# Performance work log

Hardware: AMD Instinct MI355X
Metric: run time of the kernel (lower is better)

Reference implementation:

```python
import jax, jax.numpy as jnp
import numpy as np

GATE_SLOPE = 10.0
ALPHA = 0.8
STRIDE = 1
PADDING = 1


def _unfold(x, kH, kW, stride, padding):
    # torch F.unfold equivalent, kept as (B, Cin, kH, kW, Hout, Wout)
    B, C, H, W = x.shape
    xp = jnp.pad(x, ((0, 0), (0, 0), (padding, padding), (padding, padding)))
    Hout = (H + 2 * padding - kH) // stride + 1
    Wout = (W + 2 * padding - kW) // stride + 1
    cols = []
    for i in range(kH):          # small fixed loop over kernel taps (9 iters)
        for j in range(kW):
            cols.append(xp[:, :, i:i + Hout * stride:stride, j:j + Wout * stride:stride])
    return jnp.stack(cols, axis=2).reshape(B, C, kH, kW, Hout, Wout)


def setup_inputs() -> dict:
    key = jax.random.key(0)
    ks = jax.random.split(key, 6)
    B, Cin, H, W = 4, 16, 32, 32
    Cout, K, kH, kW = 32, 3, 3, 3
    pshape = (Cout, Cin, K, kH, kW)
    x = jax.random.normal(ks[0], (B, Cin, H, W), jnp.float32)
    k = jax.random.uniform(ks[1], pshape, jnp.float32) * 2.0 + 0.5
    Ec = jax.random.uniform(ks[2], pshape, jnp.float32) * 2.0 + 0.5
    Ps = jax.random.uniform(ks[3], pshape, jnp.float32) * 1.5 + 0.5
    bias = jax.random.normal(ks[4], pshape, jnp.float32) * 0.1
    coef = jax.random.normal(ks[5], pshape, jnp.float32)
    out_bias = jnp.zeros((Cout,), jnp.float32)
    return {"x": x, "k": k, "Ec": Ec, "Ps": Ps, "bias": bias, "coef": coef, "out_bias": out_bias}


def reference(x, k, Ec, Ps, bias, coef, out_bias):
    kH, kW = k.shape[-2], k.shape[-1]
    patches = _unfold(x, kH, kW, STRIDE, PADDING)          # (B,Cin,kH,kW,Hout,Wout)
    # broadcast layout: (B, Cout, Cin, K, kH, kW, Hout, Wout)
    xe = patches[:, None, :, None]                          # (B,1,Cin,1,kH,kW,Ho,Wo)
    def bc(p):
        return p[None, :, :, :, :, :, None, None]
    k_, Ec_, Ps_, b_, c_ = bc(k), bc(Ec), bc(Ps), bc(bias), bc(coef)
    # stateless mode: prev_x = detach(x_exp) -> dx == 0 in value, grad flows via xe
    prev_x = jax.lax.stop_gradient(xe)
    is_moving_up = jax.nn.sigmoid(GATE_SLOPE * (xe - prev_x))
    crossed_pos = jax.nn.sigmoid(GATE_SLOPE * (xe - Ec_))
    crossed_neg = jax.nn.sigmoid(GATE_SLOPE * (-xe - Ec_))
    su = is_moving_up * crossed_pos
    sl = (1.0 - is_moving_up) * crossed_neg
    # branch_prev = +1 (stateless)
    target_sign = su - sl + (1.0 - su - sl)
    branch_mom = ALPHA + (1.0 - ALPHA) * target_sign
    shifted_x = xe + Ec_ * branch_mom
    basis = Ps_ * jnp.tanh(k_ * shifted_x) + b_
    out = jnp.sum(basis * c_, axis=(2, 3, 4, 5))            # (B,Cout,Hout,Wout)
    return out + out_bias[None, :, None, None]
```

## Files before the change

kernel.cpp:

```cpp
#include <hip/hip_runtime.h>


#define LOG2E 1.4426950408889634f

__global__ __launch_bounds__(256, 4) void ferro_kernel(
    const float* __restrict__ x, const float* __restrict__ k,
    const float* __restrict__ Ec, const float* __restrict__ Ps,
    const float* __restrict__ bias, const float* __restrict__ coef,
    const float* __restrict__ out_bias, float* __restrict__ out)
{
    const int bid = blockIdx.x;
    const int rb  = bid & 3;
    const int co  = (bid >> 2) & 31;
    const int b   = bid >> 7;
    const int tid = threadIdx.x;

    __shared__ float4 p4[432];
    __shared__ float  pA[432];
    __shared__ float  xs[16 * 10 * 34];
    __shared__ float  red[4];
    __shared__ float  constco_sh;

    const int pbase = co * 432;
    float cpart = 0.f;
    for (int s = tid; s < 432; s += 256) {
        float kv = k[pbase + s];
        float ev = Ec[pbase + s];
        float pv = Ps[pbase + s];
        float bv = bias[pbase + s];
        float cv = coef[pbase + s];
        float G  = 2.f * LOG2E * kv;
        float4 v;
        v.x = -10.f * LOG2E * ev;
        v.y = G;
        v.z = 0.8f * G * ev;
        v.w = 0.2f * G * ev;
        int cin = s / 27;
        int r   = s - cin * 27;
        int kk  = r / 9;
        int ij  = r - kk * 9;
        int dst = cin * 27 + ij * 3 + kk;
        p4[dst] = v;
        pA[dst] = -2.f * pv * cv;
        cpart += (pv + bv) * cv;
    }

    const int r0 = rb * 8;
    const float* xb = x + b * (16 * 32 * 32);
    for (int idx = tid; idx < 16 * 10 * 34; idx += 256) {
        int cin  = idx / 340;
        int rem  = idx - cin * 340;
        int row  = rem / 34;
        int colp = rem - row * 34;
        int gr = r0 + row - 1;
        int gc = colp - 1;
        float v = 0.f;
        if ((unsigned)gr < 32u && (unsigned)gc < 32u)
            v = xb[(cin * 32 + gr) * 32 + gc];
        xs[idx] = v;
    }

    #pragma unroll
    for (int off = 32; off > 0; off >>= 1)
        cpart += __shfl_down(cpart, off, 64);
    if ((tid & 63) == 0) red[tid >> 6] = cpart;
    __syncthreads();
    if (tid == 0) constco_sh = red[0] + red[1] + red[2] + red[3];
    __syncthreads();

    const int lr  = tid >> 5;
    const int col = tid & 31;
    const float Cx = -10.f * LOG2E;
    float acc = 0.f;

    #pragma unroll 2
    for (int cin = 0; cin < 16; ++cin) {
        const float*  xr = &xs[cin * 340 + lr * 34 + col];
        const float4* pp = &p4[cin * 27];
        const float*  aa = &pA[cin * 27];
        #pragma unroll
        for (int i = 0; i < 3; ++i) {
            #pragma unroll
            for (int j = 0; j < 3; ++j) {
                float xv = xr[i * 34 + j];
                float xC = Cx * xv;
                #pragma unroll
                for (int kk = 0; kk < 3; ++kk) {
                    int t = (i * 3 + j) * 3 + kk;
                    float4 v  = pp[t];
                    float  a2 = aa[t];
                    float e1 = __builtin_amdgcn_exp2f(xC + v.x);
                    float s  = __builtin_amdgcn_rcpf(e1 + 1.f);
                    float arg2 = fmaf(v.w, s, fmaf(v.y, xv, v.z));
                    float e2 = __builtin_amdgcn_exp2f(arg2);
                    float u  = __builtin_amdgcn_rcpf(e2 + 1.f);
                    acc = fmaf(a2, u, acc);
                }
            }
        }
    }

    float ob = out_bias[co];
    out[((b * 32 + co) * 32 + (r0 + lr)) * 32 + col] = constco_sh + acc + ob;
}

extern "C" void kernel_launch(void* const* d_in, const int* in_sizes, int n_in,
                              void* d_out, int out_size, void* d_ws, size_t ws_size,
                              hipStream_t stream) {
    const float* x        = (const float*)d_in[0];
    const float* k        = (const float*)d_in[1];
    const float* Ec       = (const float*)d_in[2];
    const float* Ps       = (const float*)d_in[3];
    const float* bias     = (const float*)d_in[4];
    const float* coef     = (const float*)d_in[5];
    const float* out_bias = (const float*)d_in[6];
    float* out = (float*)d_out;

    ferro_kernel<<<dim3(512), dim3(256), 0, stream>>>(
        x, k, Ec, Ps, bias, coef, out_bias, out);
}
```

Before: 97.04 us.

## Split parameter prep into separate kernel and split Cin across blocks with atomics

Moves per-output-channel parameter preprocessing and the constant term into a prep kernel that writes transformed parameters to workspace and initializes the output with the constant plus bias. The main kernel now splits the input channels in half across blocks, doubling the grid to 1024 blocks, and accumulates partial sums with atomicAdd. It also uses two accumulators to shorten the FMA dependency chain. This aims at better occupancy and latency hiding, at the cost of an extra launch, workspace traffic and atomic contention.

```diff
diff --git a/kernel.cpp b/kernel.cpp
--- a/kernel.cpp
+++ b/kernel.cpp
@@ -3,51 +3,90 @@
 
 #define LOG2E 1.4426950408889634f
 
-__global__ __launch_bounds__(256, 4) void ferro_kernel(
-    const float* __restrict__ x, const float* __restrict__ k,
-    const float* __restrict__ Ec, const float* __restrict__ Ps,
-    const float* __restrict__ bias, const float* __restrict__ coef,
-    const float* __restrict__ out_bias, float* __restrict__ out)
+struct WsLayout {
+};
+
+__global__ __launch_bounds__(512) void ferro_prep(
+    const float* __restrict__ k, const float* __restrict__ Ec,
+    const float* __restrict__ Ps, const float* __restrict__ bias,
+    const float* __restrict__ coef, const float* __restrict__ out_bias,
+    float4* __restrict__ p4g, float* __restrict__ pAg,
+    float* __restrict__ out)
 {
-    const int bid = blockIdx.x;
-    const int rb  = bid & 3;
-    const int co  = (bid >> 2) & 31;
-    const int b   = bid >> 7;
+    const int co  = blockIdx.x;
     const int tid = threadIdx.x;
-
-    __shared__ float4 p4[432];
-    __shared__ float  pA[432];
-    __shared__ float  xs[16 * 10 * 34];
-    __shared__ float  red[4];
-    __shared__ float  constco_sh;
+    __shared__ float red[8];
+    __shared__ float val_sh;
 
     const int pbase = co * 432;
     float cpart = 0.f;
-    for (int s = tid; s < 432; s += 256) {
-        float kv = k[pbase + s];
-        float ev = Ec[pbase + s];
-        float pv = Ps[pbase + s];
-        float bv = bias[pbase + s];
-        float cv = coef[pbase + s];
+    if (tid < 432) {
+        float kv = k[pbase + tid];
+        float ev = Ec[pbase + tid];
+        float pv = Ps[pbase + tid];
+        float bv = bias[pbase + tid];
+        float cv = coef[pbase + tid];
         float G  = 2.f * LOG2E * kv;
         float4 v;
         v.x = -10.f * LOG2E * ev;
         v.y = G;
         v.z = 0.8f * G * ev;
         v.w = 0.2f * G * ev;
-        int cin = s / 27;
-        int r   = s - cin * 27;
+        int cin = tid / 27;
+        int r   = tid - cin * 27;
         int kk  = r / 9;
         int ij  = r - kk * 9;
-        int dst = cin * 27 + ij * 3 + kk;
-        p4[dst] = v;
-        pA[dst] = -2.f * pv * cv;
-        cpart += (pv + bv) * cv;
+        int dst = pbase + cin * 27 + ij * 3 + kk;
+        p4g[dst] = v;
+        pAg[dst] = -2.f * pv * cv;
+        cpart = (pv + bv) * cv;
+    }
+    #pragma unroll
+    for (int off = 32; off > 0; off >>= 1)
+        cpart += __shfl_down(cpart, off, 64);
+    if ((tid & 63) == 0) red[tid >> 6] = cpart;
+    __syncthreads();
+    if (tid == 0) {
+        float t = 0.f;
+        #pragma unroll
+        for (int w = 0; w < 8; ++w) t += red[w];
+        val_sh = t + out_bias[co];
+    }
+    __syncthreads();
+    const float val = val_sh;
+    for (int i = tid; i < 4096; i += 512) {
+        int bI  = i >> 10;
+        int pix = i & 1023;
+        out[(bI * 32 + co) * 1024 + pix] = val;
+    }
+}
+
+__global__ __launch_bounds__(256, 4) void ferro_main(
+    const float* __restrict__ x,
+    const float4* __restrict__ p4g, const float* __restrict__ pAg,
+    float* __restrict__ out)
+{
+    const int bid  = blockIdx.x;
+    const int cinh = bid & 1;
+    const int rb   = (bid >> 1) & 3;
+    const int co   = (bid >> 3) & 31;
+    const int b    = bid >> 8;
+    const int tid  = threadIdx.x;
+
+    __shared__ float4 p4s[216];
+    __shared__ float  pAs[216];
+    __shared__ float  xs[8 * 10 * 34];
+
+    const int poff = co * 432 + cinh * 216;
+    if (tid < 216) {
+        p4s[tid] = p4g[poff + tid];
+        pAs[tid] = pAg[poff + tid];
     }
 
-    const int r0 = rb * 8;
-    const float* xb = x + b * (16 * 32 * 32);
-    for (int idx = tid; idx < 16 * 10 * 34; idx += 256) {
+    const int r0   = rb * 8;
+    const int cin0 = cinh * 8;
+    const float* xb = x + (b * 16 + cin0) * 1024;
+    for (int idx = tid; idx < 8 * 340; idx += 256) {
         int cin  = idx / 340;
         int rem  = idx - cin * 340;
         int row  = rem / 34;
@@ -59,25 +98,18 @@
             v = xb[(cin * 32 + gr) * 32 + gc];
         xs[idx] = v;
     }
-
-    #pragma unroll
-    for (int off = 32; off > 0; off >>= 1)
-        cpart += __shfl_down(cpart, off, 64);
-    if ((tid & 63) == 0) red[tid >> 6] = cpart;
-    __syncthreads();
-    if (tid == 0) constco_sh = red[0] + red[1] + red[2] + red[3];
     __syncthreads();
 
     const int lr  = tid >> 5;
     const int col = tid & 31;
     const float Cx = -10.f * LOG2E;
-    float acc = 0.f;
+    float acc0 = 0.f, acc1 = 0.f;
 
-    #pragma unroll 2
-    for (int cin = 0; cin < 16; ++cin) {
+    #pragma unroll 1
+    for (int cin = 0; cin < 8; ++cin) {
         const float*  xr = &xs[cin * 340 + lr * 34 + col];
-        const float4* pp = &p4[cin * 27];
-        const float*  aa = &pA[cin * 27];
+        const float4* pp = &p4s[cin * 27];
+        const float*  aa = &pAs[cin * 27];
         #pragma unroll
         for (int i = 0; i < 3; ++i) {
             #pragma unroll
@@ -94,14 +126,14 @@
                     float arg2 = fmaf(v.w, s, fmaf(v.y, xv, v.z));
                     float e2 = __builtin_amdgcn_exp2f(arg2);
                     float u  = __builtin_amdgcn_rcpf(e2 + 1.f);
-                    acc = fmaf(a2, u, acc);
+                    if (kk & 1) acc1 = fmaf(a2, u, acc1);
+                    else        acc0 = fmaf(a2, u, acc0);
                 }
             }
         }
     }
 
-    float ob = out_bias[co];
-    out[((b * 32 + co) * 32 + (r0 + lr)) * 32 + col] = constco_sh + acc + ob;
+    atomicAdd(&out[((b * 32 + co) * 32 + (r0 + lr)) * 32 + col], acc0 + acc1);
 }
 
 extern "C" void kernel_launch(void* const* d_in, const int* in_sizes, int n_in,
@@ -116,6 +148,10 @@
     const float* out_bias = (const float*)d_in[6];
     float* out = (float*)d_out;
 
-    ferro_kernel<<<dim3(512), dim3(256), 0, stream>>>(
-        x, k, Ec, Ps, bias, coef, out_bias, out);
+    float4* p4g = (float4*)d_ws;
+    float*  pAg = (float*)((char*)d_ws + 32 * 432 * 16);
+
+    ferro_prep<<<dim3(32), dim3(512), 0, stream>>>(
+        k, Ec, Ps, bias, coef, out_bias, p4g, pAg, out);
+    ferro_main<<<dim3(1024), dim3(256), 0, stream>>>(x, p4g, pAg, out);
 }
```

Result: faster. 93.03 us (-4.1%).

## Split input channels across half-waves and double grid to 1024 blocks

Applied to the files above, without the earlier changes.

Each block now covers 4 output rows instead of 8, which doubles the grid to 1024 blocks. Within a wave, the two 32-lane halves each handle 8 of the 16 input channels, and their partial sums are combined with a cross-lane shuffle. Each channel's inner loop keeps three independent accumulators to shorten the FMA dependency chain. This raises parallelism and instruction-level overlap on the transcendental-heavy loop. The cost is that parameter staging and the constant reduction are repeated in twice as many blocks, and half the lanes sit idle at the store.

```diff
diff --git a/kernel.cpp b/kernel.cpp
--- a/kernel.cpp
+++ b/kernel.cpp
@@ -3,23 +3,24 @@
 
 #define LOG2E 1.4426950408889634f
 
-__global__ __launch_bounds__(256, 4) void ferro_kernel(
-    const float* __restrict__ x, const float* __restrict__ k,
-    const float* __restrict__ Ec, const float* __restrict__ Ps,
-    const float* __restrict__ bias, const float* __restrict__ coef,
-    const float* __restrict__ out_bias, float* __restrict__ out)
+__global__ __launch_bounds__(256, 4) void ferro_main(
+    const float* __restrict__ x,
+    const float* __restrict__ k, const float* __restrict__ Ec,
+    const float* __restrict__ Ps, const float* __restrict__ bias,
+    const float* __restrict__ coef, const float* __restrict__ out_bias,
+    float* __restrict__ out)
 {
     const int bid = blockIdx.x;
-    const int rb  = bid & 3;
-    const int co  = (bid >> 2) & 31;
-    const int b   = bid >> 7;
+    const int rs  = bid & 7;
+    const int co  = (bid >> 3) & 31;
+    const int b   = bid >> 8;
     const int tid = threadIdx.x;
 
-    __shared__ float4 p4[432];
-    __shared__ float  pA[432];
-    __shared__ float  xs[16 * 10 * 34];
+    __shared__ float4 p4s[432];
+    __shared__ float  pAs[432];
+    __shared__ float  xs[16 * 6 * 34];
     __shared__ float  red[4];
-    __shared__ float  constco_sh;
+    __shared__ float  csh;
 
     const int pbase = co * 432;
     float cpart = 0.f;
@@ -40,19 +41,19 @@
         int kk  = r / 9;
         int ij  = r - kk * 9;
         int dst = cin * 27 + ij * 3 + kk;
-        p4[dst] = v;
-        pA[dst] = -2.f * pv * cv;
+        p4s[dst] = v;
+        pAs[dst] = -2.f * pv * cv;
         cpart += (pv + bv) * cv;
     }
 
-    const int r0 = rb * 8;
-    const float* xb = x + b * (16 * 32 * 32);
-    for (int idx = tid; idx < 16 * 10 * 34; idx += 256) {
-        int cin  = idx / 340;
-        int rem  = idx - cin * 340;
-        int row  = rem / 34;
-        int colp = rem - row * 34;
-        int gr = r0 + row - 1;
+    const int r0 = rs * 4;
+    const float* xb = x + b * (16 * 1024);
+    for (int idx = tid; idx < 16 * 204; idx += 256) {
+        int cin  = idx / 204;
+        int rem  = idx - cin * 204;
+        int row6 = rem / 34;
+        int colp = rem - row6 * 34;
+        int gr = r0 + row6 - 1;
         int gc = colp - 1;
         float v = 0.f;
         if ((unsigned)gr < 32u && (unsigned)gc < 32u)
@@ -65,43 +66,59 @@
         cpart += __shfl_down(cpart, off, 64);
     if ((tid & 63) == 0) red[tid >> 6] = cpart;
     __syncthreads();
-    if (tid == 0) constco_sh = red[0] + red[1] + red[2] + red[3];
+    if (tid == 0) csh = red[0] + red[1] + red[2] + red[3];
     __syncthreads();
 
-    const int lr  = tid >> 5;
-    const int col = tid & 31;
+    const int lane = tid & 63;
+    const int w    = tid >> 6;
+    const int col  = lane & 31;
+    const int cinh = lane >> 5;
     const float Cx = -10.f * LOG2E;
-    float acc = 0.f;
+    float acc0 = 0.f, acc1 = 0.f, acc2 = 0.f;
 
-    #pragma unroll 2
-    for (int cin = 0; cin < 16; ++cin) {
-        const float*  xr = &xs[cin * 340 + lr * 34 + col];
-        const float4* pp = &p4[cin * 27];
-        const float*  aa = &pA[cin * 27];
+    #pragma unroll 1
+    for (int c8 = 0; c8 < 8; ++c8) {
+        const int cin = cinh * 8 + c8;
+        const float*  xr = &xs[cin * 204 + w * 34 + col];
+        const float4* pp = &p4s[cin * 27];
+        const float*  aa = &pAs[cin * 27];
         #pragma unroll
-        for (int i = 0; i < 3; ++i) {
-            #pragma unroll
-            for (int j = 0; j < 3; ++j) {
-                float xv = xr[i * 34 + j];
-                float xC = Cx * xv;
-                #pragma unroll
-                for (int kk = 0; kk < 3; ++kk) {
-                    int t = (i * 3 + j) * 3 + kk;
-                    float4 v  = pp[t];
-                    float  a2 = aa[t];
-                    float e1 = __builtin_amdgcn_exp2f(xC + v.x);
-                    float s  = __builtin_amdgcn_rcpf(e1 + 1.f);
-                    float arg2 = fmaf(v.w, s, fmaf(v.y, xv, v.z));
-                    float e2 = __builtin_amdgcn_exp2f(arg2);
-                    float u  = __builtin_amdgcn_rcpf(e2 + 1.f);
-                    acc = fmaf(a2, u, acc);
-                }
+        for (int ij = 0; ij < 9; ++ij) {
+            const int i = ij / 3, j = ij - (ij / 3) * 3;
+            float xv = xr[i * 34 + j];
+            float xC = Cx * xv;
+            {
+                float4 v  = pp[ij * 3 + 0];
+                float e1 = __builtin_amdgcn_exp2f(xC + v.x);
+                float s  = __builtin_amdgcn_rcpf(e1 + 1.f);
+                float e2 = __builtin_amdgcn_exp2f(fmaf(v.w, s, fmaf(v.y, xv, v.z)));
+                float u  = __builtin_amdgcn_rcpf(e2 + 1.f);
+                acc0 = fmaf(aa[ij * 3 + 0], u, acc0);
+            }
+            {
+                float4 v  = pp[ij * 3 + 1];
+                float e1 = __builtin_amdgcn_exp2f(xC + v.x);
+                float s  = __builtin_amdgcn_rcpf(e1 + 1.f);
+                float e2 = __builtin_amdgcn_exp2f(fmaf(v.w, s, fmaf(v.y, xv, v.z)));
+                float u  = __builtin_amdgcn_rcpf(e2 + 1.f);
+                acc1 = fmaf(aa[ij * 3 + 1], u, acc1);
+            }
+            {
+                float4 v  = pp[ij * 3 + 2];
+                float e1 = __builtin_amdgcn_exp2f(xC + v.x);
+                float s  = __builtin_amdgcn_rcpf(e1 + 1.f);
+                float e2 = __builtin_amdgcn_exp2f(fmaf(v.w, s, fmaf(v.y, xv, v.z)));
+                float u  = __builtin_amdgcn_rcpf(e2 + 1.f);
+                acc2 = fmaf(aa[ij * 3 + 2], u, acc2);
             }
         }
     }
 
-    float ob = out_bias[co];
-    out[((b * 32 + co) * 32 + (r0 + lr)) * 32 + col] = constco_sh + acc + ob;
+    float acc = (acc0 + acc1) + acc2;
+    acc += __shfl_xor(acc, 32, 64);
+    if (cinh == 0) {
+        out[((b * 32 + co) * 32 + (r0 + w)) * 32 + col] = acc + csh + out_bias[co];
+    }
 }
 
 extern "C" void kernel_launch(void* const* d_in, const int* in_sizes, int n_in,
@@ -116,6 +133,6 @@
     const float* out_bias = (const float*)d_in[6];
     float* out = (float*)d_out;
 
-    ferro_kernel<<<dim3(512), dim3(256), 0, stream>>>(
+    ferro_main<<<dim3(1024), dim3(256), 0, stream>>>(
         x, k, Ec, Ps, bias, coef, out_bias, out);
 }
```

After: 91.64 us. 1.06x faster.
